# Kernel optimization log

Measured on AMD Instinct MI355X. Metric: run time of the kernel, lower is better.

## Reference

```python
import jax, jax.numpy as jnp
import numpy as np

B = 2
SPATIAL = (480, 360, 32)  # cylindrical grid (rho, phi, z) as in Cylinder3D
N = 400000
C = 32
EPS = 1e-5
NEG_SLOPE = 0.01
OFFSETS = [(d0, d2) for d0 in (-1, 0, 1) for d2 in (-1, 0, 1)]  # kernel (3,1,3)


def setup_inputs() -> dict:
    key = jax.random.key(0)
    k1, k2 = jax.random.split(key)
    # unique active voxel coordinates: sample unique linear indices then decode
    total = B * SPATIAL[0] * SPATIAL[1] * SPATIAL[2]
    rng = np.random.default_rng(0)
    lin = rng.choice(total, size=N, replace=False).astype(np.int64)
    b = lin // (SPATIAL[0] * SPATIAL[1] * SPATIAL[2])
    r = lin % (SPATIAL[0] * SPATIAL[1] * SPATIAL[2])
    c0 = r // (SPATIAL[1] * SPATIAL[2])
    r = r % (SPATIAL[1] * SPATIAL[2])
    c1 = r // SPATIAL[2]
    c2 = r % SPATIAL[2]
    coords = jnp.asarray(np.stack([b, c0, c1, c2], axis=1), dtype=jnp.int32)
    features = jax.random.normal(k1, (N, C), dtype=jnp.float32)
    weight = jax.random.normal(k2, (9, C, C), dtype=jnp.float32) * (1.0 / np.sqrt(9 * C))
    gamma = jnp.ones((C,), dtype=jnp.float32)
    beta = jnp.zeros((C,), dtype=jnp.float32)
    return {"features": features, "coords": coords, "weight": weight,
            "gamma": gamma, "beta": beta}


def _subm_conv(features, coords, weight):
    n = features.shape[0]
    # dense coordinate -> row-index lookup table (rulebook hash)
    lookup = jnp.full((B,) + SPATIAL, -1, dtype=jnp.int32)
    lookup = lookup.at[coords[:, 0], coords[:, 1], coords[:, 2], coords[:, 3]].set(
        jnp.arange(n, dtype=jnp.int32))
    out = jnp.zeros((n, weight.shape[-1]), dtype=features.dtype)
    for k, (d0, d2) in enumerate(OFFSETS):
        n0 = coords[:, 1] + d0
        n2 = coords[:, 3] + d2
        valid = (n0 >= 0) & (n0 < SPATIAL[0]) & (n2 >= 0) & (n2 < SPATIAL[2])
        nbr = lookup[coords[:, 0],
                     jnp.clip(n0, 0, SPATIAL[0] - 1),
                     coords[:, 2],
                     jnp.clip(n2, 0, SPATIAL[2] - 1)]
        nbr = jnp.where(valid, nbr, -1)
        # gather (masked) -> GEMM -> accumulate (scatter to same active sites)
        gathered = jnp.where((nbr >= 0)[:, None],
                             features[jnp.clip(nbr, 0)], 0.0)
        out = out + gathered @ weight[k]
    return out


def reference(features, coords, weight, gamma, beta):
    x = _subm_conv(features, coords, weight)          # [N, C]
    x = jnp.where(x >= 0, x, NEG_SLOPE * x)           # LeakyReLU (before BN per forward)
    mean = jnp.mean(x, axis=0)                        # BatchNorm1d, training mode
    var = jnp.mean((x - mean) ** 2, axis=0)           # biased variance
    y = (x - mean) * jax.lax.rsqrt(var + EPS) * gamma + beta
    return y
```

## Files before the change

### kernel.cpp

```cpp
#include <hip/hip_runtime.h>
#include <hip/hip_bf16.h>

#define S0 480
#define S1 360
#define S2 32
#define SLAB (S1 * S2)
#define CH 32
#define EPS 1e-5f
#define SLOPE 0.01f

#define NCOL (2 * S0 * S1)
#define SCAN_BLKS (NCOL / 256)

typedef short short8 __attribute__((ext_vector_type(8)));
typedef float f32x16 __attribute__((ext_vector_type(16)));

__device__ __forceinline__ unsigned short f2b(float f) {
    union { __hip_bfloat16 b; unsigned short u; } v;
    v.b = __float2bfloat16(f);
    return v.u;
}

__global__ __launch_bounds__(256) void scatter_or_k(
    const int4* __restrict__ coords, unsigned int* __restrict__ mask, int n)
{
    int i = blockIdx.x * 256 + threadIdx.x;
    if (i < n) {
        int4 c = coords[i];
        int col = (c.x * S0 + c.y) * S1 + c.z;
        atomicOr(&mask[col], 1u << c.w);
    }
}

__global__ __launch_bounds__(256) void scanA_k(
    const unsigned int* __restrict__ mask, int* __restrict__ bsum)
{
    int t = threadIdx.x;
    int pc = __popc(mask[blockIdx.x * 256 + t]);
#pragma unroll
    for (int m = 32; m > 0; m >>= 1) pc += __shfl_xor(pc, m, 64);
    __shared__ int red[4];
    if ((t & 63) == 0) red[t >> 6] = pc;
    __syncthreads();
    if (t == 0) bsum[blockIdx.x] = red[0] + red[1] + red[2] + red[3];
}

__global__ __launch_bounds__(256) void scanB_k(
    const int* __restrict__ bsum, int* __restrict__ bbase)
{
    const int PER = (SCAN_BLKS + 255) / 256;
    int t = threadIdx.x;
    int loc[PER];
    int tsum = 0;
#pragma unroll
    for (int j = 0; j < PER; ++j) {
        int idx = t * PER + j;
        int v = (idx < SCAN_BLKS) ? bsum[idx] : 0;
        loc[j] = v; tsum += v;
    }
    __shared__ int sa[256], sb[256];
    sa[t] = tsum; __syncthreads();
    int* src = sa; int* dst = sb;
#pragma unroll
    for (int off = 1; off < 256; off <<= 1) {
        dst[t] = src[t] + (t >= off ? src[t - off] : 0);
        __syncthreads();
        int* tmp = src; src = dst; dst = tmp;
    }
    int running = src[t] - tsum;
#pragma unroll
    for (int j = 0; j < PER; ++j) {
        int idx = t * PER + j;
        if (idx < SCAN_BLKS) { bbase[idx] = running; running += loc[j]; }
    }
}

__global__ __launch_bounds__(256) void scanC_k(
    const unsigned int* __restrict__ mask, const int* __restrict__ bbase,
    uint2* __restrict__ tab)
{
    int t = threadIdx.x;
    int col = blockIdx.x * 256 + t;
    unsigned int m = mask[col];
    int pc = __popc(m);
    __shared__ int sa[256], sb[256];
    sa[t] = pc; __syncthreads();
    int* src = sa; int* dst = sb;
#pragma unroll
    for (int off = 1; off < 256; off <<= 1) {
        dst[t] = src[t] + (t >= off ? src[t - off] : 0);
        __syncthreads();
        int* tmp = src; src = dst; dst = tmp;
    }
    int excl = src[t] - pc + bbase[blockIdx.x];
    tab[col] = make_uint2(m, (unsigned int)excl);
}

__global__ __launch_bounds__(256) void rank_k(
    const int4*  __restrict__ coords,
    const uint2* __restrict__ tab,
    uint2*       __restrict__ pinfo,
    int n)
{
    int i = blockIdx.x * 256 + threadIdx.x;
    if (i >= n) return;
    int4 c = coords[i];
    int col = (c.x * S0 + c.y) * S1 + c.z;
    int lin = col * 32 + c.w;
    uint2 tv = tab[col];
    int rank = (int)tv.y + __popc(tv.x & ((1u << c.w) - 1u));
    pinfo[rank] = make_uint2((unsigned int)i, (unsigned int)lin);
}

__global__ __launch_bounds__(256) void pack_k(
    const float* __restrict__ features,
    const uint2* __restrict__ pinfo,
    unsigned short* __restrict__ featb,
    int n)
{
    int t = threadIdx.x;
    int row = blockIdx.x * 32 + (t >> 3);
    int j = t & 7;
    if (row >= n) return;
    unsigned int orig = pinfo[row].x;
    float4 f = ((const float4*)(features + (size_t)orig * CH))[j];
    ushort4 u;
    u.x = f2b(f.x); u.y = f2b(f.y); u.z = f2b(f.z); u.w = f2b(f.w);
    ((ushort4*)(featb + (size_t)row * CH))[j] = u;
}

__global__ void bfrag_prep_k(const float* __restrict__ weight,
                             short8* __restrict__ bfrag)
{
    int lane = threadIdx.x;
    int half = lane >> 5;
    int col  = lane & 31;
#pragma unroll
    for (int t = 0; t < 9; ++t)
#pragma unroll
        for (int h = 0; h < 2; ++h) {
            short8 fr;
#pragma unroll
            for (int j = 0; j < 8; ++j) {
                int ic = h * 16 + half * 8 + j;
                fr[j] = (short)f2b(weight[t * (CH * CH) + ic * CH + col]);
            }
            bfrag[(t * 2 + h) * 64 + lane] = fr;
        }
}

__global__ __launch_bounds__(256) void conv_sorted_k(
    const unsigned short* __restrict__ featb,
    const uint2* __restrict__ pinfo,
    const uint2* __restrict__ tab,
    const short8* __restrict__ bfrag,
    unsigned short* __restrict__ xout,
    float*        __restrict__ stats_part,
    int n, int ntile)
{
    int nwg = gridDim.x;
    int bid = blockIdx.x;
    int q = nwg >> 3, r = nwg & 7;
    int xcd = bid & 7, sidx = bid >> 3;
    int blk = (xcd < r ? xcd * (q + 1) : r * (q + 1) + (xcd - r) * q) + sidx;

    int tid  = threadIdx.x;
    int lane = tid & 63;
    int wv   = tid >> 6;
    int half = lane >> 5;
    int col  = lane & 31;

    short8 B[9][2];
#pragma unroll
    for (int t = 0; t < 9; ++t) {
        B[t][0] = bfrag[(t * 2 + 0) * 64 + lane];
        B[t][1] = bfrag[(t * 2 + 1) * 64 + lane];
    }

    int tile = blk * 4 + wv;
    bool tlive = (tile < ntile);
    int p  = tile * 32 + col;
    bool live = tlive && (p < n);
    int pc = live ? p : 0;

    uint2 pi = pinfo[pc];
    int lin = (int)pi.y;
    int c2 = lin & 31;
    int colv = lin >> 5;
    int c0 = (lin / SLAB) % S0;

    int nbr[9];
#pragma unroll
    for (int d0 = 0; d0 < 3; ++d0) {
        int n0 = c0 + d0 - 1;
        bool v0 = (n0 >= 0) & (n0 < S0) & live;
        uint2 tv = v0 ? tab[colv + (d0 - 1) * S1] : make_uint2(0u, 0u);
#pragma unroll
        for (int d2 = 0; d2 < 3; ++d2) {
            int n2 = c2 + d2 - 1;
            int rk = -1;
            if (v0 && n2 >= 0 && n2 < S2 && ((tv.x >> n2) & 1u))
                rk = (int)tv.y + __popc(tv.x & ((1u << n2) - 1u));
            nbr[d0 * 3 + d2] = rk;
        }
    }

    bool act[9];
#pragma unroll
    for (int t = 0; t < 9; ++t) act[t] = (__any(nbr[t] >= 0) != 0);

    short8 A0[9], A1[9];
#pragma unroll
    for (int t = 0; t < 9; ++t) {
        short8 z;
#pragma unroll
        for (int j = 0; j < 8; ++j) z[j] = 0;
        A0[t] = z; A1[t] = z;
        int nb = nbr[t];
        if (nb >= 0) {
            const short* fp = (const short*)featb + (size_t)nb * CH;
            A0[t] = *(const short8*)(fp + half * 8);
            A1[t] = *(const short8*)(fp + 16 + half * 8);
        }
    }

    f32x16 acc;
#pragma unroll
    for (int i = 0; i < 16; ++i) acc[i] = 0.f;
#pragma unroll
    for (int t = 0; t < 9; ++t) {
        if (act[t]) {
            acc = __builtin_amdgcn_mfma_f32_32x32x16_bf16(A0[t], B[t][0], acc, 0, 0, 0);
            acc = __builtin_amdgcn_mfma_f32_32x32x16_bf16(A1[t], B[t][1], acc, 0, 0, 0);
        }
    }

    float s = 0.f, qq = 0.f;
#pragma unroll
    for (int i = 0; i < 16; ++i) {
        float v = acc[i];
        v = v >= 0.f ? v : SLOPE * v;
        int row = (i & 3) + 8 * (i >> 2) + 4 * half;
        int prow = tile * 32 + row;
        if (tlive && prow < n) {
            xout[(size_t)prow * CH + col] = f2b(v);
            s += v; qq += v * v;
        }
    }

    s  += __shfl_xor(s, 32);
    qq += __shfl_xor(qq, 32);

    __shared__ float lsum[4][32];
    __shared__ float lsq[4][32];
    if (lane < 32) { lsum[wv][col] = s; lsq[wv][col] = qq; }
    __syncthreads();
    if (tid < 32) {
        stats_part[(size_t)bid * 64 + tid] =
            lsum[0][tid] + lsum[1][tid] + lsum[2][tid] + lsum[3][tid];
    } else if (tid < 64) {
        int cc = tid - 32;
        stats_part[(size_t)bid * 64 + tid] =
            lsq[0][cc] + lsq[1][cc] + lsq[2][cc] + lsq[3][cc];
    }
}

__global__ __launch_bounds__(256) void reduce_stats_k(
    const float* __restrict__ part, float* __restrict__ stats, int nb)
{
    int c = blockIdx.x;
    float s = 0.f;
    for (int i = threadIdx.x; i < nb; i += 256)
        s += part[(size_t)i * 64 + c];
#pragma unroll
    for (int m = 32; m > 0; m >>= 1) s += __shfl_xor(s, m, 64);
    __shared__ float red[4];
    int wv = threadIdx.x >> 6;
    if ((threadIdx.x & 63) == 0) red[wv] = s;
    __syncthreads();
    if (threadIdx.x == 0) stats[c] = red[0] + red[1] + red[2] + red[3];
}

__global__ __launch_bounds__(256) void bn_apply_k(
    const unsigned short* __restrict__ xb,
    const uint2* __restrict__ pinfo,
    const float* __restrict__ stats,
    const float* __restrict__ gamma,
    const float* __restrict__ beta,
    float* __restrict__ out,
    int n)
{
    int total = n * 4;
    int stride = gridDim.x * blockDim.x;
    int g = blockIdx.x * blockDim.x + threadIdx.x;
    int c8 = g & 3;

    float scale[8], shift[8];
    float rn = 1.0f / (float)n;
#pragma unroll
    for (int j = 0; j < 8; ++j) {
        int oc = c8 * 8 + j;
        float m  = stats[oc] * rn;
        float vv = stats[CH + oc] * rn - m * m;
        float iv = rsqrtf(vv + EPS) * gamma[oc];
        scale[j] = iv;
        shift[j] = beta[oc] - m * iv;
    }

    const short8* x8 = (const short8*)xb;
    for (; g < total; g += stride) {
        int rank = g >> 2;
        unsigned int orig = pinfo[rank].x;
        short8 v = x8[g];
        float f[8];
#pragma unroll
        for (int j = 0; j < 8; ++j) {
            union { unsigned int u; float f; } w;
            w.u = ((unsigned int)(unsigned short)v[j]) << 16;
            f[j] = fmaf(w.f, scale[j], shift[j]);
        }
        float4* o = (float4*)(out + (size_t)orig * CH + c8 * 8);
        o[0] = make_float4(f[0], f[1], f[2], f[3]);
        o[1] = make_float4(f[4], f[5], f[6], f[7]);
    }
}

extern "C" void kernel_launch(void* const* d_in, const int* in_sizes, int n_in,
                              void* d_out, int out_size, void* d_ws, size_t ws_size,
                              hipStream_t stream)
{
    const float* features = (const float*)d_in[0];
    const int4*  coords   = (const int4*)d_in[1];
    const float* weight   = (const float*)d_in[2];
    const float* gamma    = (const float*)d_in[3];
    const float* beta     = (const float*)d_in[4];
    float* out = (float*)d_out;

    int n = in_sizes[0] / CH;
    int ntile = (n + 31) / 32;
    int conv_blocks = (ntile + 3) / 4;

    char* w = (char*)d_ws;
    unsigned int* mask = (unsigned int*)w;  w += (size_t)NCOL * 4;
    uint2* tab = (uint2*)w;                 w += (size_t)NCOL * 8;
    int* bsum = (int*)w;                    w += ((size_t)SCAN_BLKS * 4 + 255) & ~(size_t)255;
    int* bbase = (int*)w;                   w += ((size_t)SCAN_BLKS * 4 + 255) & ~(size_t)255;
    uint2* pinfo = (uint2*)w;               w += (size_t)n * 8;
    unsigned short* featb = (unsigned short*)w; w += (size_t)n * CH * 2;
    unsigned short* xout = (unsigned short*)w;  w += (size_t)n * CH * 2;
    float* stats_part = (float*)w;          w += (size_t)conv_blocks * 64 * 4;
    short8* bfrag = (short8*)w;             w += 9 * 2 * 64 * sizeof(short8);
    float* stats = (float*)w;

    hipMemsetAsync(mask, 0, (size_t)NCOL * 4, stream);

    scatter_or_k<<<(n + 255) / 256, 256, 0, stream>>>(coords, mask, n);
    bfrag_prep_k<<<1, 64, 0, stream>>>(weight, bfrag);
    scanA_k<<<SCAN_BLKS, 256, 0, stream>>>(mask, bsum);
    scanB_k<<<1, 256, 0, stream>>>(bsum, bbase);
    scanC_k<<<SCAN_BLKS, 256, 0, stream>>>(mask, bbase, tab);
    rank_k<<<(n + 255) / 256, 256, 0, stream>>>(coords, tab, pinfo, n);
    pack_k<<<(n + 31) / 32, 256, 0, stream>>>(features, pinfo, featb, n);

    conv_sorted_k<<<conv_blocks, 256, 0, stream>>>(
        featb, pinfo, tab, bfrag, xout, stats_part, n, ntile);

    reduce_stats_k<<<64, 256, 0, stream>>>(stats_part, stats, conv_blocks);

    bn_apply_k<<<2048, 256, 0, stream>>>(xout, pinfo, stats, gamma, beta, out, n);
}
```

Baseline: 112.8 us.

## Cut kernel launches by merging scan stages and weight prep; gather-based BN output

Folds the weight fragment preparation into the first scan kernel and merges the block-prefix scan and the local scan into one kernel. In the merged kernel each block sums all preceding block totals itself, which removes the single-block scanB launch. rank_k now also records an inverse permutation, so the BN apply kernel reads sorted rows and writes the output coalesced in original order instead of scattering. The trade-off is redundant prefix summation per block, O(blocks^2/256) reads in total, plus an extra rank array write.

```diff
diff --git a/kernel.cpp b/kernel.cpp
--- a/kernel.cpp
+++ b/kernel.cpp
@@ -33,7 +33,8 @@
 }
 
 __global__ __launch_bounds__(256) void scanA_k(
-    const unsigned int* __restrict__ mask, int* __restrict__ bsum)
+    const unsigned int* __restrict__ mask, int* __restrict__ bsum,
+    const float* __restrict__ weight, short8* __restrict__ bfrag)
 {
     int t = threadIdx.x;
     int pc = __popc(mask[blockIdx.x * 256 + t]);
@@ -43,44 +44,42 @@
     if ((t & 63) == 0) red[t >> 6] = pc;
     __syncthreads();
     if (t == 0) bsum[blockIdx.x] = red[0] + red[1] + red[2] + red[3];
-}
-
-__global__ __launch_bounds__(256) void scanB_k(
-    const int* __restrict__ bsum, int* __restrict__ bbase)
-{
-    const int PER = (SCAN_BLKS + 255) / 256;
+
+    if (blockIdx.x == 0 && t < 64) {
+        int half = t >> 5;
+        int col  = t & 31;
+#pragma unroll
+        for (int k = 0; k < 9; ++k)
+#pragma unroll
+            for (int h = 0; h < 2; ++h) {
+                short8 fr;
+#pragma unroll
+                for (int j = 0; j < 8; ++j) {
+                    int ic = h * 16 + half * 8 + j;
+                    fr[j] = (short)f2b(weight[k * (CH * CH) + ic * CH + col]);
+                }
+                bfrag[(k * 2 + h) * 64 + t] = fr;
+            }
+    }
+}
+
+__global__ __launch_bounds__(256) void scanBC_k(
+    const unsigned int* __restrict__ mask, const int* __restrict__ bsum,
+    uint2* __restrict__ tab)
+{
     int t = threadIdx.x;
-    int loc[PER];
-    int tsum = 0;
-#pragma unroll
-    for (int j = 0; j < PER; ++j) {
-        int idx = t * PER + j;
-        int v = (idx < SCAN_BLKS) ? bsum[idx] : 0;
-        loc[j] = v; tsum += v;
-    }
-    __shared__ int sa[256], sb[256];
-    sa[t] = tsum; __syncthreads();
-    int* src = sa; int* dst = sb;
-#pragma unroll
-    for (int off = 1; off < 256; off <<= 1) {
-        dst[t] = src[t] + (t >= off ? src[t - off] : 0);
-        __syncthreads();
-        int* tmp = src; src = dst; dst = tmp;
-    }
-    int running = src[t] - tsum;
-#pragma unroll
-    for (int j = 0; j < PER; ++j) {
-        int idx = t * PER + j;
-        if (idx < SCAN_BLKS) { bbase[idx] = running; running += loc[j]; }
-    }
-}
-
-__global__ __launch_bounds__(256) void scanC_k(
-    const unsigned int* __restrict__ mask, const int* __restrict__ bbase,
-    uint2* __restrict__ tab)
-{
-    int t = threadIdx.x;
-    int col = blockIdx.x * 256 + t;
+    int b = blockIdx.x;
+
+    int partial = 0;
+    for (int j = t; j < b; j += 256) partial += bsum[j];
+#pragma unroll
+    for (int m = 32; m > 0; m >>= 1) partial += __shfl_xor(partial, m, 64);
+    __shared__ int red[4];
+    if ((t & 63) == 0) red[t >> 6] = partial;
+    __syncthreads();
+    int base = red[0] + red[1] + red[2] + red[3];
+
+    int col = b * 256 + t;
     unsigned int m = mask[col];
     int pc = __popc(m);
     __shared__ int sa[256], sb[256];
@@ -92,7 +91,7 @@
         __syncthreads();
         int* tmp = src; src = dst; dst = tmp;
     }
-    int excl = src[t] - pc + bbase[blockIdx.x];
+    int excl = src[t] - pc + base;
     tab[col] = make_uint2(m, (unsigned int)excl);
 }
 
@@ -100,6 +99,7 @@
     const int4*  __restrict__ coords,
     const uint2* __restrict__ tab,
     uint2*       __restrict__ pinfo,
+    int*         __restrict__ rankof,
     int n)
 {
     int i = blockIdx.x * 256 + threadIdx.x;
@@ -110,6 +110,7 @@
     uint2 tv = tab[col];
     int rank = (int)tv.y + __popc(tv.x & ((1u << c.w) - 1u));
     pinfo[rank] = make_uint2((unsigned int)i, (unsigned int)lin);
+    rankof[i] = rank;
 }
 
 __global__ __launch_bounds__(256) void pack_k(
@@ -127,26 +128,6 @@
     ushort4 u;
     u.x = f2b(f.x); u.y = f2b(f.y); u.z = f2b(f.z); u.w = f2b(f.w);
     ((ushort4*)(featb + (size_t)row * CH))[j] = u;
-}
-
-__global__ void bfrag_prep_k(const float* __restrict__ weight,
-                             short8* __restrict__ bfrag)
-{
-    int lane = threadIdx.x;
-    int half = lane >> 5;
-    int col  = lane & 31;
-#pragma unroll
-    for (int t = 0; t < 9; ++t)
-#pragma unroll
-        for (int h = 0; h < 2; ++h) {
-            short8 fr;
-#pragma unroll
-            for (int j = 0; j < 8; ++j) {
-                int ic = h * 16 + half * 8 + j;
-                fr[j] = (short)f2b(weight[t * (CH * CH) + ic * CH + col]);
-            }
-            bfrag[(t * 2 + h) * 64 + lane] = fr;
-        }
 }
 
 __global__ __launch_bounds__(256) void conv_sorted_k(
@@ -281,9 +262,9 @@
     if (threadIdx.x == 0) stats[c] = red[0] + red[1] + red[2] + red[3];
 }
 
-__global__ __launch_bounds__(256) void bn_apply_k(
+__global__ __launch_bounds__(256) void bn_gather_k(
     const unsigned short* __restrict__ xb,
-    const uint2* __restrict__ pinfo,
+    const int*   __restrict__ rankof,
     const float* __restrict__ stats,
     const float* __restrict__ gamma,
     const float* __restrict__ beta,
@@ -309,9 +290,9 @@
 
     const short8* x8 = (const short8*)xb;
     for (; g < total; g += stride) {
-        int rank = g >> 2;
-        unsigned int orig = pinfo[rank].x;
-        short8 v = x8[g];
+        int i = g >> 2;
+        int rank = rankof[i];
+        short8 v = x8[(size_t)rank * 4 + c8];
         float f[8];
 #pragma unroll
         for (int j = 0; j < 8; ++j) {
@@ -319,7 +300,7 @@
             w.u = ((unsigned int)(unsigned short)v[j]) << 16;
             f[j] = fmaf(w.f, scale[j], shift[j]);
         }
-        float4* o = (float4*)(out + (size_t)orig * CH + c8 * 8);
+        float4* o = (float4*)(out + (size_t)i * CH + c8 * 8);
         o[0] = make_float4(f[0], f[1], f[2], f[3]);
         o[1] = make_float4(f[4], f[5], f[6], f[7]);
     }
@@ -344,8 +325,8 @@
     unsigned int* mask = (unsigned int*)w;  w += (size_t)NCOL * 4;
     uint2* tab = (uint2*)w;                 w += (size_t)NCOL * 8;
     int* bsum = (int*)w;                    w += ((size_t)SCAN_BLKS * 4 + 255) & ~(size_t)255;
-    int* bbase = (int*)w;                   w += ((size_t)SCAN_BLKS * 4 + 255) & ~(size_t)255;
     uint2* pinfo = (uint2*)w;               w += (size_t)n * 8;
+    int* rankof = (int*)w;                  w += (size_t)n * 4;
     unsigned short* featb = (unsigned short*)w; w += (size_t)n * CH * 2;
     unsigned short* xout = (unsigned short*)w;  w += (size_t)n * CH * 2;
     float* stats_part = (float*)w;          w += (size_t)conv_blocks * 64 * 4;
@@ -355,11 +336,9 @@
     hipMemsetAsync(mask, 0, (size_t)NCOL * 4, stream);
 
     scatter_or_k<<<(n + 255) / 256, 256, 0, stream>>>(coords, mask, n);
-    bfrag_prep_k<<<1, 64, 0, stream>>>(weight, bfrag);
-    scanA_k<<<SCAN_BLKS, 256, 0, stream>>>(mask, bsum);
-    scanB_k<<<1, 256, 0, stream>>>(bsum, bbase);
-    scanC_k<<<SCAN_BLKS, 256, 0, stream>>>(mask, bbase, tab);
-    rank_k<<<(n + 255) / 256, 256, 0, stream>>>(coords, tab, pinfo, n);
+    scanA_k<<<SCAN_BLKS, 256, 0, stream>>>(mask, bsum, weight, bfrag);
+    scanBC_k<<<SCAN_BLKS, 256, 0, stream>>>(mask, bsum, tab);
+    rank_k<<<(n + 255) / 256, 256, 0, stream>>>(coords, tab, pinfo, rankof, n);
     pack_k<<<(n + 31) / 32, 256, 0, stream>>>(features, pinfo, featb, n);
 
     conv_sorted_k<<<conv_blocks, 256, 0, stream>>>(
@@ -367,5 +346,5 @@
 
     reduce_stats_k<<<64, 256, 0, stream>>>(stats_part, stats, conv_blocks);
 
-    bn_apply_k<<<2048, 256, 0, stream>>>(xout, pinfo, stats, gamma, beta, out, n);
-}
+    bn_gather_k<<<2048, 256, 0, stream>>>(xout, rankof, stats, gamma, beta, out, n);
+}
```

New measurement: 112.6 us. About the same (-0.2%).
